# Optimization experiments

Measured on AMD Instinct MI355X. Metric: run time of the kernel, lower is better.

The kernel has to match this reference:

```python
import jax, jax.numpy as jnp
import numpy as np

N = 20000        # genes
E = 100000       # edges per relation
D_IN = 512
HID = 64         # hidden_dim (per-head channels in layers 0,1)
HEADS = 8
D_H = HID * HEADS   # 512 hidden width
D_OUT = 256
NEG_SLOPE = 0.2  # GATv2Conv default negative_slope


def _gatv2(x, src, dst, Wl, bl, Wr, br, att, out_bias, heads, ch):
    """PyG GATv2Conv, add_self_loops=False, concat=True, eval mode (no dropout)."""
    n = x.shape[0]
    xl = (x @ Wl + bl).reshape(n, heads, ch)   # lin_l (source transform)
    xr = (x @ Wr + br).reshape(n, heads, ch)   # lin_r (target transform)
    e = jax.nn.leaky_relu(xl[src] + xr[dst], NEG_SLOPE)   # [E,H,C]
    score = jnp.einsum('ehc,hc->eh', e, att)              # [E,H]
    # segment softmax over incoming edges of each destination node
    m = jax.ops.segment_max(score, dst, num_segments=n)   # [N,H]
    w = jnp.exp(score - m[dst])
    z = jax.ops.segment_sum(w, dst, num_segments=n)
    alpha = w / z[dst]
    out = jax.ops.segment_sum(alpha[:, :, None] * xl[src], dst, num_segments=n)
    return out.reshape(n, heads * ch) + out_bias


def _layernorm(x, g, b):
    mu = x.mean(-1, keepdims=True)
    var = x.var(-1, keepdims=True)
    return (x - mu) * jax.lax.rsqrt(var + 1e-5) * g + b


def setup_inputs() -> dict:
    key = jax.random.key(0)
    ks = jax.random.split(key, 12)
    gn = lambda k, shape, fan_in: (jax.random.normal(k, shape, dtype=jnp.float32)
                                   / np.float32(np.sqrt(fan_in)))
    inp = {}
    inp['x'] = jax.random.normal(ks[0], (N, D_IN), dtype=jnp.float32)
    inp['edge_index'] = jax.random.randint(ks[1], (3, 2, E), 0, N, dtype=jnp.int32)
    # input projection  Linear(512 -> 512)
    inp['proj_w'] = gn(ks[2], (D_IN, D_H), D_IN)
    inp['proj_b'] = jnp.zeros((D_H,), jnp.float32)
    # layers 0,1: stacked over [layer, edge_type]
    inp['l01_lin_l_w'] = gn(ks[3], (2, 3, D_H, D_H), D_H)
    inp['l01_lin_l_b'] = jnp.zeros((2, 3, D_H), jnp.float32)
    inp['l01_lin_r_w'] = gn(ks[4], (2, 3, D_H, D_H), D_H)
    inp['l01_lin_r_b'] = jnp.zeros((2, 3, D_H), jnp.float32)
    inp['l01_att'] = gn(ks[5], (2, 3, HEADS, HID), HID)
    inp['l01_bias'] = jnp.zeros((2, 3, D_H), jnp.float32)
    # layer 2: heads=1, out_channels=256, stacked over edge_type
    inp['l2_lin_l_w'] = gn(ks[6], (3, D_H, D_OUT), D_H)
    inp['l2_lin_l_b'] = jnp.zeros((3, D_OUT), jnp.float32)
    inp['l2_lin_r_w'] = gn(ks[7], (3, D_H, D_OUT), D_H)
    inp['l2_lin_r_b'] = jnp.zeros((3, D_OUT), jnp.float32)
    inp['l2_att'] = gn(ks[8], (3, 1, D_OUT), D_OUT)
    inp['l2_bias'] = jnp.zeros((3, D_OUT), jnp.float32)
    # LayerNorms
    inp['ln01_gamma'] = jnp.ones((2, D_H), jnp.float32)
    inp['ln01_beta'] = jnp.zeros((2, D_H), jnp.float32)
    inp['ln2_gamma'] = jnp.ones((D_OUT,), jnp.float32)
    inp['ln2_beta'] = jnp.zeros((D_OUT,), jnp.float32)
    return inp


def reference(x, edge_index, proj_w, proj_b,
              l01_lin_l_w, l01_lin_l_b, l01_lin_r_w, l01_lin_r_b, l01_att, l01_bias,
              l2_lin_l_w, l2_lin_l_b, l2_lin_r_w, l2_lin_r_b, l2_att, l2_bias,
              ln01_gamma, ln01_beta, ln2_gamma, ln2_beta):
    # input proj + ELU (dropout = identity in eval)
    h = jax.nn.elu(x @ proj_w + proj_b)
    # layers 0 and 1: HeteroConv(sum over 3 relations), ELU, residual, LayerNorm
    for li in range(2):
        res = h
        out = 0.0
        for et in range(3):
            src, dst = edge_index[et, 0], edge_index[et, 1]
            out = out + _gatv2(h, src, dst,
                               l01_lin_l_w[li, et], l01_lin_l_b[li, et],
                               l01_lin_r_w[li, et], l01_lin_r_b[li, et],
                               l01_att[li, et], l01_bias[li, et], HEADS, HID)
        h = jax.nn.elu(out) + res
        h = _layernorm(h, ln01_gamma[li], ln01_beta[li])
    # layer 2: heads=1, out=256; no residual (dims differ)
    out = 0.0
    for et in range(3):
        src, dst = edge_index[et, 0], edge_index[et, 1]
        out = out + _gatv2(h, src, dst,
                           l2_lin_l_w[et], l2_lin_l_b[et],
                           l2_lin_r_w[et], l2_lin_r_b[et],
                           l2_att[et], l2_bias[et], 1, D_OUT)
    h = jax.nn.elu(out)
    return _layernorm(h, ln2_gamma, ln2_beta)
```

## Files before the change

kernel.cpp:

```cpp
#include <hip/hip_runtime.h>


#define NN 20000
#define NE 100000
#define DH 512
#define DOUT 256

typedef __attribute__((ext_vector_type(8))) short short8;
typedef __attribute__((ext_vector_type(4))) short short4v;
typedef __attribute__((ext_vector_type(4))) float f32x4;

__device__ __forceinline__ float b2f(unsigned short s) {
    union { unsigned u; float f; } v; v.u = ((unsigned)s) << 16; return v.f;
}
__device__ __forceinline__ unsigned short f2b(float f) {
    unsigned u = __float_as_uint(f);
    u += 0x7FFFu + ((u >> 16) & 1u);
    return (unsigned short)(u >> 16);
}
__device__ __forceinline__ void load_lds16(const unsigned short* g, unsigned short* l) {
    __builtin_amdgcn_global_load_lds(
        (const __attribute__((address_space(1))) unsigned int*)g,
        (__attribute__((address_space(3))) unsigned int*)l, 16, 0, 0);
}

__global__ void cvt_f2b_k(const float* __restrict__ in,
                          unsigned short* __restrict__ out, int n) {
    int i0 = (blockIdx.x * blockDim.x + threadIdx.x) * 8;
    if (i0 >= n) return;
    #pragma unroll
    for (int j = 0; j < 8; j++) out[i0 + j] = f2b(in[i0 + j]);
}

struct TSeg { const float* in; unsigned short* out; int C; };
struct TTable { TSeg s[19]; };

__global__ void transpose_all_k(TTable t) {
    __shared__ float tile[32][33];
    TSeg d = t.s[blockIdx.y];
    int tiles_x = d.C >> 5;
    int nt = tiles_x << 4;
    if ((int)blockIdx.x >= nt) return;
    int bx = blockIdx.x % tiles_x, by = blockIdx.x / tiles_x;
    int c0 = bx * 32, r0 = by * 32;
    int tx = threadIdx.x & 31, ty = threadIdx.x >> 5;
    #pragma unroll
    for (int i = ty; i < 32; i += 8)
        tile[i][tx] = d.in[(size_t)(r0 + i) * d.C + c0 + tx];
    __syncthreads();
    #pragma unroll
    for (int i = ty; i < 32; i += 8)
        d.out[(size_t)(c0 + i) * 512 + r0 + tx] = f2b(tile[tx][i]);
}

__global__ void count_all_k(const int* __restrict__ ei, int* __restrict__ counts) {
    int i = blockIdx.x * blockDim.x + threadIdx.x;
    if (i >= 3 * NE) return;
    int et = i / NE, idx = i - et * NE;
    int d = ei[(size_t)et * 2 * NE + NE + idx];
    atomicAdd(&counts[et * (NN + 1) + d], 1);
}

__global__ __launch_bounds__(1024)
void scan_par_k(const int* __restrict__ counts, int* __restrict__ offs, int n) {
    __shared__ int part[1024];
    const int* c = counts + (size_t)blockIdx.x * (n + 1);
    int* o = offs + (size_t)blockIdx.x * (n + 1);
    int tid = threadIdx.x;
    int per = (n + 1023) / 1024;
    int base = tid * per;
    int lim = min(base + per, n);
    int sum = 0;
    for (int i = base; i < lim; i++) sum += c[i];
    part[tid] = sum;
    __syncthreads();
    #pragma unroll
    for (int off = 1; off < 1024; off <<= 1) {
        int v = (tid >= off) ? part[tid - off] : 0;
        __syncthreads();
        part[tid] += v;
        __syncthreads();
    }
    int run = part[tid] - sum;
    for (int i = base; i < lim; i++) { o[i] = run; run += c[i]; }
    if (tid == 1023) o[n] = part[1023];
}

__global__ void scatter_all_k(const int* __restrict__ ei, int* __restrict__ cursor,
                              int* __restrict__ srcs_sorted) {
    int i = blockIdx.x * blockDim.x + threadIdx.x;
    if (i >= 3 * NE) return;
    int et = i / NE, idx = i - et * NE;
    int s = ei[(size_t)et * 2 * NE + idx];
    int d = ei[(size_t)et * 2 * NE + NE + idx];
    int p = atomicAdd(&cursor[et * (NN + 1) + d], 1);
    srcs_sorted[(size_t)et * NE + p] = s;
}

template<int ACT, int SEGL2>
__global__ __launch_bounds__(256)
void gemm_k(const unsigned short* __restrict__ A,
            const unsigned short* __restrict__ Bt,
            const float* __restrict__ lb,
            const float* __restrict__ rb,
            unsigned short* __restrict__ Cb,
            int M, int N, int K, int MT, int NT, int STRIPE) {
    __shared__ __align__(16) unsigned short smem[17408];
    unsigned short* As = smem;
    unsigned short* Bs = smem + 8192;
    int bid = blockIdx.x;
    int xcd = bid & 7, r = bid >> 3;
    int mtile = xcd * STRIPE + r / NT;
    int ntile = r % NT;
    if (mtile >= MT) return;
    int bm0 = mtile * 128, bn0 = ntile * 128;

    int tid = threadIdx.x;
    int lane = tid & 63, wave = tid >> 6;
    int quad = lane >> 4, l16 = lane & 15;
    int rw = (wave >> 1) * 64, cw = (wave & 1) * 64;
    int rxor = l16 & 7;

    f32x4 acc[4][4];
    #pragma unroll
    for (int mi = 0; mi < 4; mi++)
        #pragma unroll
        for (int ni = 0; ni < 4; ni++) acc[mi][ni] = (f32x4){0.f, 0.f, 0.f, 0.f};

    for (int k0 = 0; k0 < K; k0 += 64) {
        #pragma unroll
        for (int i = 0; i < 4; i++) {
            int f = i * 256 + tid;
            int row = f >> 3, s = f & 7;
            int cg = s ^ (row & 7);
            load_lds16(A + (size_t)(bm0 + row) * K + k0 + cg * 8, As + f * 8);
        }
        #pragma unroll
        for (int i = 0; i < 4; i++) {
            int f = i * 256 + tid;
            int col = f >> 3, s = f & 7;
            int cg = s ^ (col & 7);
            load_lds16(Bt + (size_t)(bn0 + col) * K + k0 + cg * 8, Bs + f * 8);
        }
        __syncthreads();
        #pragma unroll
        for (int ki = 0; ki < 64; ki += 32) {
            int kch = quad + (ki >> 3);
            int slot = kch ^ rxor;
            short8 af[4], bf[4];
            #pragma unroll
            for (int mi = 0; mi < 4; mi++)
                af[mi] = *(const short8*)(As + (rw + mi * 16 + l16) * 64 + slot * 8);
            #pragma unroll
            for (int ni = 0; ni < 4; ni++)
                bf[ni] = *(const short8*)(Bs + (cw + ni * 16 + l16) * 64 + slot * 8);
            #pragma unroll
            for (int mi = 0; mi < 4; mi++)
                #pragma unroll
                for (int ni = 0; ni < 4; ni++)
                    acc[mi][ni] = __builtin_amdgcn_mfma_f32_16x16x32_bf16(
                        af[mi], bf[ni], acc[mi][ni], 0, 0, 0);
        }
        __syncthreads();
    }

    #pragma unroll
    for (int ni = 0; ni < 4; ni++) {
        int col = cw + ni * 16 + l16;
        int seg = col >> (SEGL2 + 1);
        int lr = (col >> SEGL2) & 1;
        int cc2 = col & ((1 << SEGL2) - 1);
        float bv = (lr ? rb : lb)[(seg << SEGL2) + cc2];
        #pragma unroll
        for (int mi = 0; mi < 4; mi++) {
            int row = rw + mi * 16 + quad * 4;
            #pragma unroll
            for (int i = 0; i < 4; i++) {
                float v = acc[mi][ni][i] + bv;
                if (ACT == 1) v = v > 0.f ? v : expm1f(v);
                smem[(row + i) * 136 + col] = f2b(v);
            }
        }
    }
    __syncthreads();
    #pragma unroll
    for (int it = 0; it < 8; it++) {
        int chunk = it * 256 + tid;
        int row = chunk >> 4, cc = chunk & 15;
        int grow = bm0 + row;
        if (grow < M) {
            uint4 d = *(const uint4*)(smem + row * 136 + cc * 8);
            *(uint4*)(Cb + (size_t)grow * N + bn0 + cc * 8) = d;
        }
    }
}

#define MMAC(AF, P)                                                         \
    __builtin_amdgcn_s_setprio(1);                                          \
    _Pragma("unroll")                                                       \
    for (int mi = 0; mi < 2; mi++)                                          \
        _Pragma("unroll")                                                   \
        for (int nn = 0; nn < 4; nn++)                                      \
            _Pragma("unroll")                                               \
            for (int s2 = 0; s2 < 2; s2++)                                  \
                acc[2 * (P) + mi][nn] = __builtin_amdgcn_mfma_f32_16x16x32_bf16( \
                    AF[mi][s2], bfr[nn][s2], acc[2 * (P) + mi][nn], 0, 0, 0); \
    __builtin_amdgcn_s_setprio(0);

template<int ACT, int SEGL2>
__global__ __launch_bounds__(512, 2)
void gemm256_k(const unsigned short* __restrict__ A,
               const unsigned short* __restrict__ Bt,
               const float* __restrict__ lb,
               const float* __restrict__ rb,
               unsigned short* __restrict__ Cb,
               int M, int N, int K, int MT, int NT) {
    __shared__ __align__(16) unsigned short smem[65536];

    int bid = blockIdx.x;
    int nwg = MT * NT;
    int q = nwg >> 3, r = nwg & 7;
    int xcd = bid & 7;
    int wg = (xcd < r ? xcd * (q + 1) : r * (q + 1) + (xcd - r) * q) + (bid >> 3);
    int mtile = wg / NT, ntile = wg % NT;
    int bm0 = mtile * 256, bn0 = ntile * 256;

    int tid = threadIdx.x;
    int lane = tid & 63, wid = tid >> 6;
    int wr = wid >> 2, wc = wid & 3;
    int quad = lane >> 4, l16 = lane & 15;
    int rbase = wr * 128, cbase = wc * 64;
    int rxor = l16 & 7;

    f32x4 acc[8][4];
    #pragma unroll
    for (int m = 0; m < 8; m++)
        #pragma unroll
        for (int n = 0; n < 4; n++) acc[m][n] = (f32x4){0.f, 0.f, 0.f, 0.f};

    const int NKT = K >> 6;

    auto stage2 = [&](int grp, int kt1) {
        unsigned short* Asw = smem + (kt1 & 1) * 32768;
        unsigned short* Bsw = Asw + 16384;
        int kk = kt1 << 6;
        int f = grp * 512 + tid;
        int row = f >> 3, s = f & 7;
        int cg = s ^ (row & 7);
        load_lds16(A + (size_t)(bm0 + row) * K + kk + cg * 8, Asw + f * 8);
        load_lds16(Bt + (size_t)(bn0 + row) * K + kk + cg * 8, Bsw + f * 8);
    };
    auto readA = [&](short8 (&dst)[2][2], const unsigned short* Asr, int p) {
        #pragma unroll
        for (int mi = 0; mi < 2; mi++)
            #pragma unroll
            for (int s2 = 0; s2 < 2; s2++)
                dst[mi][s2] = *(const short8*)(Asr +
                    (rbase + (2 * p + mi) * 16 + l16) * 64 +
                    ((quad + s2 * 4) ^ rxor) * 8);
    };

    stage2(0, 0); stage2(1, 0); stage2(2, 0); stage2(3, 0);
    __syncthreads();

    short8 afA[2][2], afB[2][2], bfr[4][2];
    {
        const unsigned short* A0 = smem;
        const unsigned short* B0 = smem + 16384;
        #pragma unroll
        for (int n = 0; n < 4; n++)
            #pragma unroll
            for (int s2 = 0; s2 < 2; s2++)
                bfr[n][s2] = *(const short8*)(B0 +
                    (cbase + n * 16 + l16) * 64 + ((quad + s2 * 4) ^ rxor) * 8);
        readA(afA, A0, 0);
    }

    for (int kt = 0; kt < NKT; kt++) {
        const unsigned short* Asr = smem + (kt & 1) * 32768;
        bool st = (kt + 1 < NKT);

        if (st) { stage2(0, kt + 1); stage2(1, kt + 1); }
        __builtin_amdgcn_sched_barrier(0);
        readA(afB, Asr, 1);
        MMAC(afA, 0)
        if (st) { stage2(2, kt + 1); stage2(3, kt + 1); }
        __builtin_amdgcn_sched_barrier(0);
        readA(afA, Asr, 2);
        MMAC(afB, 1)
        readA(afB, Asr, 3);
        MMAC(afA, 2)
        MMAC(afB, 3)

        __syncthreads();

        if (st) {
            const unsigned short* An = smem + ((kt + 1) & 1) * 32768;
            const unsigned short* Bn = An + 16384;
            #pragma unroll
            for (int n = 0; n < 4; n++)
                #pragma unroll
                for (int s2 = 0; s2 < 2; s2++)
                    bfr[n][s2] = *(const short8*)(Bn +
                        (cbase + n * 16 + l16) * 64 + ((quad + s2 * 4) ^ rxor) * 8);
            readA(afA, An, 0);
        }
    }

    #pragma unroll
    for (int h = 0; h < 2; h++) {
        __syncthreads();
        if (wr == h) {
            #pragma unroll
            for (int n = 0; n < 4; n++) {
                int col = cbase + n * 16 + l16;
                int gcol = bn0 + col;
                int seg = gcol >> (SEGL2 + 1);
                int lr = (gcol >> SEGL2) & 1;
                int cc2 = gcol & ((1 << SEGL2) - 1);
                float bv = (lr ? rb : lb)[(seg << SEGL2) + cc2];
                #pragma unroll
                for (int m = 0; m < 8; m++) {
                    int lrow = m * 16 + quad * 4;
                    #pragma unroll
                    for (int i = 0; i < 4; i++) {
                        float v = acc[m][n][i] + bv;
                        if (ACT == 1) v = v > 0.f ? v : expm1f(v);
                        smem[(lrow + i) * 264 + col] = f2b(v);
                    }
                }
            }
        }
        __syncthreads();
        #pragma unroll
        for (int it = 0; it < 8; it++) {
            int chunk = it * 512 + tid;
            int row = chunk >> 5, cc = chunk & 31;
            int grow = bm0 + h * 128 + row;
            if (grow < M) {
                uint4 d = *(const uint4*)(smem + row * 264 + cc * 8);
                *(uint4*)(Cb + (size_t)grow * N + bn0 + cc * 8) = d;
            }
        }
    }
}

__global__ __launch_bounds__(192)
void gat_fused01_k(const unsigned short* __restrict__ C,
                   const int* __restrict__ offs3,
                   const int* __restrict__ srcs3,
                   const float* __restrict__ att,
                   const float* __restrict__ bias3,
                   unsigned short* __restrict__ hb,
                   const float* __restrict__ gamma,
                   const float* __restrict__ beta,
                   int n_nodes) {
    const unsigned LD = 3072;
    __shared__ float lds_tot[2 * DH];
    int tid = threadIdx.x;
    int lane = tid & 63, et = tid >> 6;
    int n = blockIdx.x;
    int c0 = lane * 8;

    const int* offs = offs3 + et * (NN + 1);
    const int* srcs = srcs3 + (size_t)et * NE;
    int e0 = offs[n], e1 = offs[n + 1];

    float tot[8];
    #pragma unroll
    for (int j = 0; j < 8; j++) tot[j] = 0.f;

    if (e0 < e1) {
        const unsigned short* XL = C + et * 1024 + c0;
        float xr[8], at[8];
        {
            short8 t = *(const short8*)(C + (size_t)n * LD + et * 1024 + 512 + c0);
            #pragma unroll
            for (int j = 0; j < 8; j++) xr[j] = b2f((unsigned short)t[j]);
            #pragma unroll
            for (int j = 0; j < 8; j++) at[j] = att[et * 512 + c0 + j];
        }
        float z = 0.f;
        float acc[8];
        #pragma unroll
        for (int j = 0; j < 8; j++) acc[j] = 0.f;

        auto G = [&](int idx) {
            return *(const short8*)(XL + (unsigned)srcs[idx] * LD);
        };
        auto process = [&](short8 cur) {
            float xl[8];
            #pragma unroll
            for (int j = 0; j < 8; j++) xl[j] = b2f((unsigned short)cur[j]);
            float p = 0.f;
            #pragma unroll
            for (int j = 0; j < 8; j++) {
                float v = xl[j] + xr[j];
                v = fmaxf(v, 0.2f * v);
                p = fmaf(v, at[j], p);
            }
            p += __shfl_xor(p, 1, 64);
            p += __shfl_xor(p, 2, 64);
            p += __shfl_xor(p, 4, 64);
            float wgt = __expf(p);
            z += wgt;
            #pragma unroll
            for (int j = 0; j < 8; j++) acc[j] = fmaf(wgt, xl[j], acc[j]);
        };

        int ef = e0, eb = e1 - 1;
        short8 a0 = G(ef);
        short8 a1 = G(min(ef + 1, eb));
        short8 b0 = G(eb);
        short8 b1 = G(max(eb - 1, ef));
        while (ef < eb) {
            short8 ca = a0; a0 = a1; a1 = G(min(ef + 2, eb));
            short8 cb = b0; b0 = b1; b1 = G(max(eb - 2, ef));
            process(ca);
            process(cb);
            ef++; eb--;
        }
        if (ef == eb) process(a0);

        float inv = 1.f / z;
        #pragma unroll
        for (int j = 0; j < 8; j++) tot[j] = acc[j] * inv;
    }

    if (et) {
        float* dst = lds_tot + (et - 1) * DH + lane;
        #pragma unroll
        for (int j = 0; j < 8; j++) dst[j * 64] = tot[j];
    }
    __syncthreads();
    if (et == 0) {
        unsigned short* hrow = hb + (size_t)n * DH + c0;
        short8 rt = *(const short8*)hrow;
        float v[8];
        float s1 = 0.f;
        #pragma unroll
        for (int j = 0; j < 8; j++) {
            int c = c0 + j;
            float x = tot[j] + lds_tot[j * 64 + lane] + lds_tot[DH + j * 64 + lane]
                    + bias3[c] + bias3[512 + c] + bias3[1024 + c];
            x = x > 0.f ? x : expm1f(x);
            x += b2f((unsigned short)rt[j]);
            v[j] = x;
            s1 += x;
        }
        #pragma unroll
        for (int off = 1; off < 64; off <<= 1) s1 += __shfl_xor(s1, off, 64);
        float mean = s1 * (1.f / DH);
        float s2 = 0.f;
        #pragma unroll
        for (int j = 0; j < 8; j++) { float d = v[j] - mean; s2 += d * d; }
        #pragma unroll
        for (int off = 1; off < 64; off <<= 1) s2 += __shfl_xor(s2, off, 64);
        float rstd = rsqrtf(s2 * (1.f / DH) + 1e-5f);
        short8 ov;
        #pragma unroll
        for (int j = 0; j < 8; j++) {
            int c = c0 + j;
            ov[j] = (short)f2b((v[j] - mean) * rstd * gamma[c] + beta[c]);
        }
        *(short8*)hrow = ov;
    }
    (void)n_nodes;
}

__global__ __launch_bounds__(192)
void gat_fused2_k(const unsigned short* __restrict__ C,
                  const int* __restrict__ offs3,
                  const int* __restrict__ srcs3,
                  const float* __restrict__ att,
                  const float* __restrict__ bias3,
                  const float* __restrict__ gamma,
                  const float* __restrict__ beta,
                  float* __restrict__ out, int n_nodes) {
    const unsigned LD = 1536;
    __shared__ float lds_tot[2 * DOUT];
    int tid = threadIdx.x;
    int lane = tid & 63, et = tid >> 6;
    int n = blockIdx.x;
    int c0 = lane * 4;

    const int* offs = offs3 + et * (NN + 1);
    const int* srcs = srcs3 + (size_t)et * NE;
    int e0 = offs[n], e1 = offs[n + 1];

    float tot[4] = {0.f, 0.f, 0.f, 0.f};

    if (e0 < e1) {
        const unsigned short* XL = C + et * 512 + c0;
        float xr[4], at[4];
        {
            short4v t = *(const short4v*)(C + (size_t)n * LD + et * 512 + 256 + c0);
            #pragma unroll
            for (int j = 0; j < 4; j++) xr[j] = b2f((unsigned short)t[j]);
            #pragma unroll
            for (int j = 0; j < 4; j++) at[j] = att[et * 256 + c0 + j];
        }
        float z = 0.f;
        float acc[4] = {0.f, 0.f, 0.f, 0.f};

        auto G = [&](int idx) {
            return *(const short4v*)(XL + (unsigned)srcs[idx] * LD);
        };
        auto process = [&](short4v cur) {
            float xl[4];
            #pragma unroll
            for (int j = 0; j < 4; j++) xl[j] = b2f((unsigned short)cur[j]);
            float p = 0.f;
            #pragma unroll
            for (int j = 0; j < 4; j++) {
                float v = xl[j] + xr[j];
                v = fmaxf(v, 0.2f * v);
                p = fmaf(v, at[j], p);
            }
            #pragma unroll
            for (int off = 1; off < 64; off <<= 1) p += __shfl_xor(p, off, 64);
            float wgt = __expf(p);
            z += wgt;
            #pragma unroll
            for (int j = 0; j < 4; j++) acc[j] = fmaf(wgt, xl[j], acc[j]);
        };

        int ef = e0, eb = e1 - 1;
        short4v a0 = G(ef);
        short4v a1 = G(min(ef + 1, eb));
        short4v b0 = G(eb);
        short4v b1 = G(max(eb - 1, ef));
        while (ef < eb) {
            short4v ca = a0; a0 = a1; a1 = G(min(ef + 2, eb));
            short4v cb = b0; b0 = b1; b1 = G(max(eb - 2, ef));
            process(ca);
            process(cb);
            ef++; eb--;
        }
        if (ef == eb) process(a0);

        float inv = 1.f / z;
        #pragma unroll
        for (int j = 0; j < 4; j++) tot[j] = acc[j] * inv;
    }

    if (et) {
        float* dst = lds_tot + (et - 1) * DOUT + lane;
        #pragma unroll
        for (int j = 0; j < 4; j++) dst[j * 64] = tot[j];
    }
    __syncthreads();
    if (et == 0) {
        float v[4];
        float s1 = 0.f;
        #pragma unroll
        for (int j = 0; j < 4; j++) {
            int c = c0 + j;
            float x = tot[j] + lds_tot[j * 64 + lane] + lds_tot[DOUT + j * 64 + lane]
                    + bias3[c] + bias3[256 + c] + bias3[512 + c];
            x = x > 0.f ? x : expm1f(x);
            v[j] = x;
            s1 += x;
        }
        #pragma unroll
        for (int off = 1; off < 64; off <<= 1) s1 += __shfl_xor(s1, off, 64);
        float mean = s1 * (1.f / DOUT);
        float s2 = 0.f;
        #pragma unroll
        for (int j = 0; j < 4; j++) { float d = v[j] - mean; s2 += d * d; }
        #pragma unroll
        for (int off = 1; off < 64; off <<= 1) s2 += __shfl_xor(s2, off, 64);
        float rstd = rsqrtf(s2 * (1.f / DOUT) + 1e-5f);
        f32x4 o;
        #pragma unroll
        for (int j = 0; j < 4; j++) {
            int c = c0 + j;
            o[j] = (v[j] - mean) * rstd * gamma[c] + beta[c];
        }
        *(f32x4*)(out + (size_t)n * DOUT + c0) = o;
    }
    (void)n_nodes;
}

extern "C" void kernel_launch(void* const* d_in, const int* in_sizes, int n_in,
                              void* d_out, int out_size, void* d_ws, size_t ws_size,
                              hipStream_t stream) {
    const float* x       = (const float*)d_in[0];
    const int*   ei      = (const int*)d_in[1];
    const float* proj_w  = (const float*)d_in[2];
    const float* proj_b  = (const float*)d_in[3];
    const float* l01lw   = (const float*)d_in[4];
    const float* l01lb   = (const float*)d_in[5];
    const float* l01rw   = (const float*)d_in[6];
    const float* l01rb   = (const float*)d_in[7];
    const float* l01att  = (const float*)d_in[8];
    const float* l01bias = (const float*)d_in[9];
    const float* l2lw    = (const float*)d_in[10];
    const float* l2lb    = (const float*)d_in[11];
    const float* l2rw    = (const float*)d_in[12];
    const float* l2rb    = (const float*)d_in[13];
    const float* l2att   = (const float*)d_in[14];
    const float* l2bias  = (const float*)d_in[15];
    const float* g01     = (const float*)d_in[16];
    const float* b01     = (const float*)d_in[17];
    const float* g2      = (const float*)d_in[18];
    const float* b2      = (const float*)d_in[19];
    (void)in_sizes; (void)n_in; (void)out_size; (void)ws_size;

    char* w = (char*)d_ws;
    size_t off = 0;
    auto carve = [&](size_t bytes) { void* p = w + off; off = (off + bytes + 255) & ~(size_t)255; return p; };
    unsigned short* h_b     = (unsigned short*)carve((size_t)NN * DH * 2);
    unsigned short* xb      = (unsigned short*)carve((size_t)NN * DH * 2);
    unsigned short* Cbuf    = (unsigned short*)carve((size_t)NN * 3072 * 2);
    unsigned short* Wt      = (unsigned short*)carve((size_t)4194304 * 2);
    int*            counts3 = (int*)           carve((size_t)3 * (NN + 1) * 4);
    int*            offs3   = (int*)           carve((size_t)3 * (NN + 1) * 4);
    int*            srcs3   = (int*)           carve((size_t)3 * NE * 4);
    carve(65536);

    unsigned short* Wt_proj = Wt;
    unsigned short* Wt_L0   = Wt_proj + 262144;
    unsigned short* Wt_L1   = Wt_L0 + 3072 * 512;
    unsigned short* Wt_L2   = Wt_L1 + 3072 * 512;

    dim3 tb(256);
    const int MT  = (NN + 255) / 256;
    const int MT1 = (NN + 127) / 128;
    const int STRIPE1 = (MT1 + 7) / 8;

    cvt_f2b_k<<<dim3(5000), tb, 0, stream>>>(x, xb, NN * DH);
    TTable tt;
    {
        int s = 0;
        tt.s[s++] = {proj_w, Wt_proj, 512};
        for (int li = 0; li < 2; li++) {
            unsigned short* base = li ? Wt_L1 : Wt_L0;
            for (int et = 0; et < 3; et++)
                tt.s[s++] = {l01lw + (size_t)(li * 3 + et) * 262144,
                             base + (size_t)et * 2 * 262144, 512};
            for (int et = 0; et < 3; et++)
                tt.s[s++] = {l01rw + (size_t)(li * 3 + et) * 262144,
                             base + 262144 + (size_t)et * 2 * 262144, 512};
        }
        for (int et = 0; et < 3; et++)
            tt.s[s++] = {l2lw + (size_t)et * 131072,
                         Wt_L2 + (size_t)et * 2 * 131072, 256};
        for (int et = 0; et < 3; et++)
            tt.s[s++] = {l2rw + (size_t)et * 131072,
                         Wt_L2 + 131072 + (size_t)et * 2 * 131072, 256};
    }
    transpose_all_k<<<dim3(256, 19), tb, 0, stream>>>(tt);

    hipMemsetAsync(counts3, 0, (size_t)3 * (NN + 1) * 4, stream);
    count_all_k<<<dim3((3 * NE + 255) / 256), tb, 0, stream>>>(ei, counts3);
    scan_par_k<<<dim3(3), dim3(1024), 0, stream>>>(counts3, offs3, NN);
    hipMemcpyAsync(counts3, offs3, (size_t)3 * (NN + 1) * 4,
                   hipMemcpyDeviceToDevice, stream);
    scatter_all_k<<<dim3((3 * NE + 255) / 256), tb, 0, stream>>>(ei, counts3, srcs3);

    gemm_k<1, 9><<<dim3(8 * STRIPE1 * 4), tb, 0, stream>>>(
        xb, Wt_proj, proj_b, proj_b, h_b, NN, 512, 512, MT1, 4, STRIPE1);

    for (int li = 0; li < 2; li++) {
        gemm256_k<0, 9><<<dim3(MT * 12), dim3(512), 0, stream>>>(
            h_b, li ? Wt_L1 : Wt_L0,
            l01lb + (size_t)li * 3 * 512, l01rb + (size_t)li * 3 * 512,
            Cbuf, NN, 3072, 512, MT, 12);
        gat_fused01_k<<<dim3(NN), dim3(192), 0, stream>>>(
            Cbuf, offs3, srcs3,
            l01att + (size_t)li * 3 * 512, l01bias + (size_t)li * 3 * 512,
            h_b, g01 + (size_t)li * DH, b01 + (size_t)li * DH, NN);
    }

    gemm_k<0, 8><<<dim3(8 * STRIPE1 * 12), tb, 0, stream>>>(
        h_b, Wt_L2, l2lb, l2rb, Cbuf, NN, 1536, 512, MT1, 12, STRIPE1);
    gat_fused2_k<<<dim3(NN), dim3(192), 0, stream>>>(
        Cbuf, offs3, srcs3, l2att, l2bias, g2, b2, (float*)d_out, NN);
}
```

Before: 659.4 us.

## Merge per-relation edge lists into one node-major list, one wave per node

Edges of all three relations are now sorted into a single node-major array that stores src*3+et, so one wavefront walks all incoming edges of a node across relations and uses a single running prefetch pipeline. This removes the LDS reduction and __syncthreads between the three per-relation wavefronts, and packs four nodes per 256-thread block. A small cursor-init kernel replaces the device memcpy. The trade-off is serial processing of the three relations within one wave, which lowers per-node parallelism and makes the gather addressing depend on the C layout (row stride 1024 per node-relation).

```diff
diff --git a/kernel.cpp b/kernel.cpp
--- a/kernel.cpp
+++ b/kernel.cpp
@@ -7,7 +7,6 @@
 #define DOUT 256
 
 typedef __attribute__((ext_vector_type(8))) short short8;
-typedef __attribute__((ext_vector_type(4))) short short4v;
 typedef __attribute__((ext_vector_type(4))) float f32x4;
 
 __device__ __forceinline__ float b2f(unsigned short s) {
@@ -86,15 +85,28 @@
     if (tid == 1023) o[n] = part[1023];
 }
 
+__global__ void cursor_init_k(const int* __restrict__ offs3,
+                              int* __restrict__ cur3) {
+    int n = blockIdx.x * blockDim.x + threadIdx.x;
+    if (n >= NN) return;
+    int o0a = offs3[n],                o0b = offs3[n + 1];
+    int o1a = offs3[(NN + 1) + n],     o1b = offs3[(NN + 1) + n + 1];
+    int o2a = offs3[2 * (NN + 1) + n];
+    int S = o0a + o1a + o2a;
+    cur3[n]          = S;
+    cur3[NN + n]     = S + (o0b - o0a);
+    cur3[2 * NN + n] = S + (o0b - o0a) + (o1b - o1a);
+}
+
 __global__ void scatter_all_k(const int* __restrict__ ei, int* __restrict__ cursor,
-                              int* __restrict__ srcs_sorted) {
+                              int* __restrict__ srcm) {
     int i = blockIdx.x * blockDim.x + threadIdx.x;
     if (i >= 3 * NE) return;
     int et = i / NE, idx = i - et * NE;
     int s = ei[(size_t)et * 2 * NE + idx];
     int d = ei[(size_t)et * 2 * NE + NE + idx];
-    int p = atomicAdd(&cursor[et * (NN + 1) + d], 1);
-    srcs_sorted[(size_t)et * NE + p] = s;
+    int p = atomicAdd(&cursor[et * NN + d], 1);
+    srcm[p] = s * 3 + et;
 }
 
 template<int ACT, int SEGL2>
@@ -345,241 +357,229 @@
     }
 }
 
-__global__ __launch_bounds__(192)
+__global__ __launch_bounds__(256)
 void gat_fused01_k(const unsigned short* __restrict__ C,
                    const int* __restrict__ offs3,
-                   const int* __restrict__ srcs3,
+                   const int* __restrict__ srcm,
                    const float* __restrict__ att,
                    const float* __restrict__ bias3,
                    unsigned short* __restrict__ hb,
                    const float* __restrict__ gamma,
                    const float* __restrict__ beta,
                    int n_nodes) {
-    const unsigned LD = 3072;
-    __shared__ float lds_tot[2 * DH];
     int tid = threadIdx.x;
-    int lane = tid & 63, et = tid >> 6;
-    int n = blockIdx.x;
-    int c0 = lane * 8;
-
-    const int* offs = offs3 + et * (NN + 1);
-    const int* srcs = srcs3 + (size_t)et * NE;
-    int e0 = offs[n], e1 = offs[n + 1];
+    int lane = tid & 63;
+    int n = blockIdx.x * 4 + (tid >> 6);
+    if (n >= n_nodes) return;
+    int cl = lane * 8;
+    const unsigned short* Cl = C + cl;
+
+    int o0a = offs3[n],                o0b = offs3[n + 1];
+    int o1a = offs3[(NN + 1) + n],     o1b = offs3[(NN + 1) + n + 1];
+    int o2a = offs3[2 * (NN + 1) + n], o2b = offs3[2 * (NN + 1) + n + 1];
+    int S = o0a + o1a + o2a;
+    int b1 = S + (o0b - o0a);
+    int b2 = b1 + (o1b - o1a);
+    int E = b2 + (o2b - o2a);
 
     float tot[8];
     #pragma unroll
     for (int j = 0; j < 8; j++) tot[j] = 0.f;
 
-    if (e0 < e1) {
-        const unsigned short* XL = C + et * 1024 + c0;
+    if (S < E) {
+        int last = E - 1;
+        auto G = [&](int i) {
+            return *(const uint4*)(Cl + (size_t)(unsigned)srcm[i] * 1024);
+        };
+        uint4 p0 = G(S);
+        uint4 p1 = G(min(S + 1, last));
+        uint4 p2 = G(min(S + 2, last));
+        int e = S;
         float xr[8], at[8];
-        {
-            short8 t = *(const short8*)(C + (size_t)n * LD + et * 1024 + 512 + c0);
-            #pragma unroll
-            for (int j = 0; j < 8; j++) xr[j] = b2f((unsigned short)t[j]);
-            #pragma unroll
-            for (int j = 0; j < 8; j++) at[j] = att[et * 512 + c0 + j];
-        }
-        float z = 0.f;
-        float acc[8];
-        #pragma unroll
-        for (int j = 0; j < 8; j++) acc[j] = 0.f;
-
-        auto G = [&](int idx) {
-            return *(const short8*)(XL + (unsigned)srcs[idx] * LD);
-        };
-        auto process = [&](short8 cur) {
-            float xl[8];
-            #pragma unroll
-            for (int j = 0; j < 8; j++) xl[j] = b2f((unsigned short)cur[j]);
-            float p = 0.f;
-            #pragma unroll
-            for (int j = 0; j < 8; j++) {
-                float v = xl[j] + xr[j];
-                v = fmaxf(v, 0.2f * v);
-                p = fmaf(v, at[j], p);
+
+        #pragma unroll
+        for (int et = 0; et < 3; et++) {
+            int segend = (et == 0) ? b1 : ((et == 1) ? b2 : E);
+            if (e < segend) {
+                {
+                    short8 t = *(const short8*)(C + (size_t)(n * 3 + et) * 1024 + 512 + cl);
+                    #pragma unroll
+                    for (int j = 0; j < 8; j++) xr[j] = b2f((unsigned short)t[j]);
+                    #pragma unroll
+                    for (int j = 0; j < 8; j++) at[j] = att[et * 512 + cl + j];
+                }
+                float z = 0.f, acc[8];
+                #pragma unroll
+                for (int j = 0; j < 8; j++) acc[j] = 0.f;
+                for (; e < segend; e++) {
+                    uint4 cur = p0; p0 = p1; p1 = p2; p2 = G(min(e + 3, last));
+                    float xl[8];
+                    xl[0] = __uint_as_float(cur.x << 16);
+                    xl[1] = __uint_as_float(cur.x & 0xffff0000u);
+                    xl[2] = __uint_as_float(cur.y << 16);
+                    xl[3] = __uint_as_float(cur.y & 0xffff0000u);
+                    xl[4] = __uint_as_float(cur.z << 16);
+                    xl[5] = __uint_as_float(cur.z & 0xffff0000u);
+                    xl[6] = __uint_as_float(cur.w << 16);
+                    xl[7] = __uint_as_float(cur.w & 0xffff0000u);
+                    float p = 0.f;
+                    #pragma unroll
+                    for (int j = 0; j < 8; j++) {
+                        float v = xl[j] + xr[j];
+                        v = fmaxf(v, 0.2f * v);
+                        p = fmaf(v, at[j], p);
+                    }
+                    p += __shfl_xor(p, 1, 64);
+                    p += __shfl_xor(p, 2, 64);
+                    p += __shfl_xor(p, 4, 64);
+                    float wgt = __expf(p);
+                    z += wgt;
+                    #pragma unroll
+                    for (int j = 0; j < 8; j++) acc[j] = fmaf(wgt, xl[j], acc[j]);
+                }
+                float inv = 1.f / z;
+                #pragma unroll
+                for (int j = 0; j < 8; j++) tot[j] = fmaf(acc[j], inv, tot[j]);
             }
-            p += __shfl_xor(p, 1, 64);
-            p += __shfl_xor(p, 2, 64);
-            p += __shfl_xor(p, 4, 64);
-            float wgt = __expf(p);
-            z += wgt;
-            #pragma unroll
-            for (int j = 0; j < 8; j++) acc[j] = fmaf(wgt, xl[j], acc[j]);
-        };
-
-        int ef = e0, eb = e1 - 1;
-        short8 a0 = G(ef);
-        short8 a1 = G(min(ef + 1, eb));
-        short8 b0 = G(eb);
-        short8 b1 = G(max(eb - 1, ef));
-        while (ef < eb) {
-            short8 ca = a0; a0 = a1; a1 = G(min(ef + 2, eb));
-            short8 cb = b0; b0 = b1; b1 = G(max(eb - 2, ef));
-            process(ca);
-            process(cb);
-            ef++; eb--;
-        }
-        if (ef == eb) process(a0);
-
-        float inv = 1.f / z;
-        #pragma unroll
-        for (int j = 0; j < 8; j++) tot[j] = acc[j] * inv;
-    }
-
-    if (et) {
-        float* dst = lds_tot + (et - 1) * DH + lane;
-        #pragma unroll
-        for (int j = 0; j < 8; j++) dst[j * 64] = tot[j];
-    }
-    __syncthreads();
-    if (et == 0) {
-        unsigned short* hrow = hb + (size_t)n * DH + c0;
-        short8 rt = *(const short8*)hrow;
-        float v[8];
-        float s1 = 0.f;
-        #pragma unroll
-        for (int j = 0; j < 8; j++) {
-            int c = c0 + j;
-            float x = tot[j] + lds_tot[j * 64 + lane] + lds_tot[DH + j * 64 + lane]
-                    + bias3[c] + bias3[512 + c] + bias3[1024 + c];
-            x = x > 0.f ? x : expm1f(x);
-            x += b2f((unsigned short)rt[j]);
-            v[j] = x;
-            s1 += x;
-        }
-        #pragma unroll
-        for (int off = 1; off < 64; off <<= 1) s1 += __shfl_xor(s1, off, 64);
-        float mean = s1 * (1.f / DH);
-        float s2 = 0.f;
-        #pragma unroll
-        for (int j = 0; j < 8; j++) { float d = v[j] - mean; s2 += d * d; }
-        #pragma unroll
-        for (int off = 1; off < 64; off <<= 1) s2 += __shfl_xor(s2, off, 64);
-        float rstd = rsqrtf(s2 * (1.f / DH) + 1e-5f);
-        short8 ov;
-        #pragma unroll
-        for (int j = 0; j < 8; j++) {
-            int c = c0 + j;
-            ov[j] = (short)f2b((v[j] - mean) * rstd * gamma[c] + beta[c]);
-        }
-        *(short8*)hrow = ov;
-    }
-    (void)n_nodes;
-}
-
-__global__ __launch_bounds__(192)
+        }
+    }
+
+    unsigned short* hrow = hb + (size_t)n * DH + cl;
+    short8 rt = *(const short8*)hrow;
+    float v[8];
+    float s1 = 0.f;
+    #pragma unroll
+    for (int j = 0; j < 8; j++) {
+        int c = cl + j;
+        float x = tot[j] + bias3[c] + bias3[512 + c] + bias3[1024 + c];
+        x = x > 0.f ? x : expm1f(x);
+        x += b2f((unsigned short)rt[j]);
+        v[j] = x;
+        s1 += x;
+    }
+    #pragma unroll
+    for (int off = 1; off < 64; off <<= 1) s1 += __shfl_xor(s1, off, 64);
+    float mean = s1 * (1.f / DH);
+    float s2 = 0.f;
+    #pragma unroll
+    for (int j = 0; j < 8; j++) { float d = v[j] - mean; s2 += d * d; }
+    #pragma unroll
+    for (int off = 1; off < 64; off <<= 1) s2 += __shfl_xor(s2, off, 64);
+    float rstd = rsqrtf(s2 * (1.f / DH) + 1e-5f);
+    short8 ov;
+    #pragma unroll
+    for (int j = 0; j < 8; j++) {
+        int c = cl + j;
+        ov[j] = (short)f2b((v[j] - mean) * rstd * gamma[c] + beta[c]);
+    }
+    *(short8*)hrow = ov;
+}
+
+__global__ __launch_bounds__(256)
 void gat_fused2_k(const unsigned short* __restrict__ C,
                   const int* __restrict__ offs3,
-                  const int* __restrict__ srcs3,
+                  const int* __restrict__ srcm,
                   const float* __restrict__ att,
                   const float* __restrict__ bias3,
                   const float* __restrict__ gamma,
                   const float* __restrict__ beta,
                   float* __restrict__ out, int n_nodes) {
-    const unsigned LD = 1536;
-    __shared__ float lds_tot[2 * DOUT];
     int tid = threadIdx.x;
-    int lane = tid & 63, et = tid >> 6;
-    int n = blockIdx.x;
-    int c0 = lane * 4;
-
-    const int* offs = offs3 + et * (NN + 1);
-    const int* srcs = srcs3 + (size_t)et * NE;
-    int e0 = offs[n], e1 = offs[n + 1];
+    int lane = tid & 63;
+    int n = blockIdx.x * 4 + (tid >> 6);
+    if (n >= n_nodes) return;
+    int cl = lane * 4;
+    const unsigned short* Cl = C + cl;
+
+    int o0a = offs3[n],                o0b = offs3[n + 1];
+    int o1a = offs3[(NN + 1) + n],     o1b = offs3[(NN + 1) + n + 1];
+    int o2a = offs3[2 * (NN + 1) + n], o2b = offs3[2 * (NN + 1) + n + 1];
+    int S = o0a + o1a + o2a;
+    int b1 = S + (o0b - o0a);
+    int b2 = b1 + (o1b - o1a);
+    int E = b2 + (o2b - o2a);
 
     float tot[4] = {0.f, 0.f, 0.f, 0.f};
 
-    if (e0 < e1) {
-        const unsigned short* XL = C + et * 512 + c0;
+    if (S < E) {
+        int last = E - 1;
+        auto G = [&](int i) {
+            return *(const uint2*)(Cl + (size_t)(unsigned)srcm[i] * 512);
+        };
+        uint2 p0 = G(S);
+        uint2 p1 = G(min(S + 1, last));
+        uint2 p2 = G(min(S + 2, last));
+        int e = S;
         float xr[4], at[4];
-        {
-            short4v t = *(const short4v*)(C + (size_t)n * LD + et * 512 + 256 + c0);
-            #pragma unroll
-            for (int j = 0; j < 4; j++) xr[j] = b2f((unsigned short)t[j]);
-            #pragma unroll
-            for (int j = 0; j < 4; j++) at[j] = att[et * 256 + c0 + j];
-        }
-        float z = 0.f;
-        float acc[4] = {0.f, 0.f, 0.f, 0.f};
-
-        auto G = [&](int idx) {
-            return *(const short4v*)(XL + (unsigned)srcs[idx] * LD);
-        };
-        auto process = [&](short4v cur) {
-            float xl[4];
-            #pragma unroll
-            for (int j = 0; j < 4; j++) xl[j] = b2f((unsigned short)cur[j]);
-            float p = 0.f;
-            #pragma unroll
-            for (int j = 0; j < 4; j++) {
-                float v = xl[j] + xr[j];
-                v = fmaxf(v, 0.2f * v);
-                p = fmaf(v, at[j], p);
+
+        #pragma unroll
+        for (int et = 0; et < 3; et++) {
+            int segend = (et == 0) ? b1 : ((et == 1) ? b2 : E);
+            if (e < segend) {
+                {
+                    const unsigned short* xrp = C + (size_t)(n * 3 + et) * 512 + 256 + cl;
+                    #pragma unroll
+                    for (int j = 0; j < 4; j++) xr[j] = b2f(xrp[j]);
+                    #pragma unroll
+                    for (int j = 0; j < 4; j++) at[j] = att[et * 256 + cl + j];
+                }
+                float z = 0.f, acc[4];
+                #pragma unroll
+                for (int j = 0; j < 4; j++) acc[j] = 0.f;
+                for (; e < segend; e++) {
+                    uint2 cur = p0; p0 = p1; p1 = p2; p2 = G(min(e + 3, last));
+                    float xl[4];
+                    xl[0] = __uint_as_float(cur.x << 16);
+                    xl[1] = __uint_as_float(cur.x & 0xffff0000u);
+                    xl[2] = __uint_as_float(cur.y << 16);
+                    xl[3] = __uint_as_float(cur.y & 0xffff0000u);
+                    float p = 0.f;
+                    #pragma unroll
+                    for (int j = 0; j < 4; j++) {
+                        float v = xl[j] + xr[j];
+                        v = fmaxf(v, 0.2f * v);
+                        p = fmaf(v, at[j], p);
+                    }
+                    #pragma unroll
+                    for (int off = 1; off < 64; off <<= 1) p += __shfl_xor(p, off, 64);
+                    float wgt = __expf(p);
+                    z += wgt;
+                    #pragma unroll
+                    for (int j = 0; j < 4; j++) acc[j] = fmaf(wgt, xl[j], acc[j]);
+                }
+                float inv = 1.f / z;
+                #pragma unroll
+                for (int j = 0; j < 4; j++) tot[j] = fmaf(acc[j], inv, tot[j]);
             }
-            #pragma unroll
-            for (int off = 1; off < 64; off <<= 1) p += __shfl_xor(p, off, 64);
-            float wgt = __expf(p);
-            z += wgt;
-            #pragma unroll
-            for (int j = 0; j < 4; j++) acc[j] = fmaf(wgt, xl[j], acc[j]);
-        };
-
-        int ef = e0, eb = e1 - 1;
-        short4v a0 = G(ef);
-        short4v a1 = G(min(ef + 1, eb));
-        short4v b0 = G(eb);
-        short4v b1 = G(max(eb - 1, ef));
-        while (ef < eb) {
-            short4v ca = a0; a0 = a1; a1 = G(min(ef + 2, eb));
-            short4v cb = b0; b0 = b1; b1 = G(max(eb - 2, ef));
-            process(ca);
-            process(cb);
-            ef++; eb--;
-        }
-        if (ef == eb) process(a0);
-
-        float inv = 1.f / z;
-        #pragma unroll
-        for (int j = 0; j < 4; j++) tot[j] = acc[j] * inv;
-    }
-
-    if (et) {
-        float* dst = lds_tot + (et - 1) * DOUT + lane;
-        #pragma unroll
-        for (int j = 0; j < 4; j++) dst[j * 64] = tot[j];
-    }
-    __syncthreads();
-    if (et == 0) {
-        float v[4];
-        float s1 = 0.f;
-        #pragma unroll
-        for (int j = 0; j < 4; j++) {
-            int c = c0 + j;
-            float x = tot[j] + lds_tot[j * 64 + lane] + lds_tot[DOUT + j * 64 + lane]
-                    + bias3[c] + bias3[256 + c] + bias3[512 + c];
-            x = x > 0.f ? x : expm1f(x);
-            v[j] = x;
-            s1 += x;
-        }
-        #pragma unroll
-        for (int off = 1; off < 64; off <<= 1) s1 += __shfl_xor(s1, off, 64);
-        float mean = s1 * (1.f / DOUT);
-        float s2 = 0.f;
-        #pragma unroll
-        for (int j = 0; j < 4; j++) { float d = v[j] - mean; s2 += d * d; }
-        #pragma unroll
-        for (int off = 1; off < 64; off <<= 1) s2 += __shfl_xor(s2, off, 64);
-        float rstd = rsqrtf(s2 * (1.f / DOUT) + 1e-5f);
-        f32x4 o;
-        #pragma unroll
-        for (int j = 0; j < 4; j++) {
-            int c = c0 + j;
-            o[j] = (v[j] - mean) * rstd * gamma[c] + beta[c];
-        }
-        *(f32x4*)(out + (size_t)n * DOUT + c0) = o;
-    }
-    (void)n_nodes;
+        }
+    }
+
+    float v[4];
+    float s1 = 0.f;
+    #pragma unroll
+    for (int j = 0; j < 4; j++) {
+        int c = cl + j;
+        float x = tot[j] + bias3[c] + bias3[256 + c] + bias3[512 + c];
+        x = x > 0.f ? x : expm1f(x);
+        v[j] = x;
+        s1 += x;
+    }
+    #pragma unroll
+    for (int off = 1; off < 64; off <<= 1) s1 += __shfl_xor(s1, off, 64);
+    float mean = s1 * (1.f / DOUT);
+    float s2 = 0.f;
+    #pragma unroll
+    for (int j = 0; j < 4; j++) { float d = v[j] - mean; s2 += d * d; }
+    #pragma unroll
+    for (int off = 1; off < 64; off <<= 1) s2 += __shfl_xor(s2, off, 64);
+    float rstd = rsqrtf(s2 * (1.f / DOUT) + 1e-5f);
+    f32x4 o;
+    #pragma unroll
+    for (int j = 0; j < 4; j++) {
+        int c = cl + j;
+        o[j] = (v[j] - mean) * rstd * gamma[c] + beta[c];
+    }
+    *(f32x4*)(out + (size_t)n * DOUT + cl) = o;
 }
 
 extern "C" void kernel_launch(void* const* d_in, const int* in_sizes, int n_in,
@@ -616,7 +616,7 @@
     unsigned short* Wt      = (unsigned short*)carve((size_t)4194304 * 2);
     int*            counts3 = (int*)           carve((size_t)3 * (NN + 1) * 4);
     int*            offs3   = (int*)           carve((size_t)3 * (NN + 1) * 4);
-    int*            srcs3   = (int*)           carve((size_t)3 * NE * 4);
+    int*            srcm    = (int*)           carve((size_t)3 * NE * 4);
     carve(65536);
 
     unsigned short* Wt_proj = Wt;
@@ -655,9 +655,8 @@
     hipMemsetAsync(counts3, 0, (size_t)3 * (NN + 1) * 4, stream);
     count_all_k<<<dim3((3 * NE + 255) / 256), tb, 0, stream>>>(ei, counts3);
     scan_par_k<<<dim3(3), dim3(1024), 0, stream>>>(counts3, offs3, NN);
-    hipMemcpyAsync(counts3, offs3, (size_t)3 * (NN + 1) * 4,
-                   hipMemcpyDeviceToDevice, stream);
-    scatter_all_k<<<dim3((3 * NE + 255) / 256), tb, 0, stream>>>(ei, counts3, srcs3);
+    cursor_init_k<<<dim3((NN + 255) / 256), tb, 0, stream>>>(offs3, counts3);
+    scatter_all_k<<<dim3((3 * NE + 255) / 256), tb, 0, stream>>>(ei, counts3, srcm);
 
     gemm_k<1, 9><<<dim3(8 * STRIPE1 * 4), tb, 0, stream>>>(
         xb, Wt_proj, proj_b, proj_b, h_b, NN, 512, 512, MT1, 4, STRIPE1);
@@ -667,14 +666,14 @@
             h_b, li ? Wt_L1 : Wt_L0,
             l01lb + (size_t)li * 3 * 512, l01rb + (size_t)li * 3 * 512,
             Cbuf, NN, 3072, 512, MT, 12);
-        gat_fused01_k<<<dim3(NN), dim3(192), 0, stream>>>(
-            Cbuf, offs3, srcs3,
+        gat_fused01_k<<<dim3(NN / 4), tb, 0, stream>>>(
+            Cbuf, offs3, srcm,
             l01att + (size_t)li * 3 * 512, l01bias + (size_t)li * 3 * 512,
             h_b, g01 + (size_t)li * DH, b01 + (size_t)li * DH, NN);
     }
 
     gemm_k<0, 8><<<dim3(8 * STRIPE1 * 12), tb, 0, stream>>>(
         h_b, Wt_L2, l2lb, l2rb, Cbuf, NN, 1536, 512, MT1, 12, STRIPE1);
-    gat_fused2_k<<<dim3(NN), dim3(192), 0, stream>>>(
-        Cbuf, offs3, srcs3, l2att, l2bias, g2, b2, (float*)d_out, NN);
-}
+    gat_fused2_k<<<dim3(NN / 4), tb, 0, stream>>>(
+        Cbuf, offs3, srcm, l2att, l2bias, g2, b2, (float*)d_out, NN);
+}
```

Result: slower. 679.1 us (+3.0%).
